# Kernel tuning notes

Hardware: AMD Instinct MI355X
Metric: run time of the kernel (lower is better)

Reference implementation:

```python
import jax, jax.numpy as jnp
import numpy as np

B, L, S, D_MODEL, H = 2, 2048, 2048, 1024, 16
D_HEAD = D_MODEL // H  # 64


def setup_inputs() -> dict:
    key = jax.random.key(0)
    ks = jax.random.split(key, 11)
    s = 0.02
    return {
        "queries": jax.random.normal(ks[0], (B, L, D_MODEL), jnp.float32),
        "keys": jax.random.normal(ks[1], (B, S, D_MODEL), jnp.float32),
        "values": jax.random.normal(ks[2], (B, S, D_MODEL), jnp.float32),
        # Linear weights stored as [in, out] (torch W.T), biases [out]
        "Wq": jax.random.normal(ks[3], (D_MODEL, H * D_HEAD), jnp.float32) * s,
        "bq": jnp.zeros((H * D_HEAD,), jnp.float32),
        "Wk": jax.random.normal(ks[4], (D_MODEL, H * D_HEAD), jnp.float32) * s,
        "bk": jnp.zeros((H * D_HEAD,), jnp.float32),
        "Wv": jax.random.normal(ks[5], (D_MODEL, H * D_HEAD), jnp.float32) * s,
        "bv": jnp.zeros((H * D_HEAD,), jnp.float32),
        "Wo": jax.random.normal(ks[6], (H * D_HEAD, D_MODEL), jnp.float32) * s,
        "bo": jnp.zeros((D_MODEL,), jnp.float32),
    }


def reference(queries, keys, values, Wq, bq, Wk, bk, Wv, bv, Wo, bo):
    b, l, _ = queries.shape
    _, s, _ = keys.shape
    # QKV projections -> [B, L/S, H, D_HEAD]
    q = (queries @ Wq + bq).reshape(b, l, H, D_HEAD)
    k = (keys @ Wk + bk).reshape(b, s, H, D_HEAD)
    v = (values @ Wv + bv).reshape(b, s, H, D_HEAD)
    scale = 1.0 / jnp.sqrt(jnp.asarray(D_HEAD, q.dtype))
    # Full score matrix [B, H, L, S] (mask_flag=False -> no causal mask)
    scores = jnp.einsum("blhe,bshe->bhls", q, k)
    A = jax.nn.softmax(scale * scores, axis=-1)  # dropout is identity at eval
    out = jnp.einsum("bhls,bshd->blhd", A, v).reshape(b, l, H * D_HEAD)
    out = out @ Wo + bo
    return out, A
```

## Files before the change

kernel.cpp:

```cpp
#include <hip/hip_runtime.h>


typedef __attribute__((ext_vector_type(8))) __bf16 bf16x8;
typedef __attribute__((ext_vector_type(4))) float f32x4;

__device__ __forceinline__ unsigned int f2bf_u(float f) {
  unsigned int u = __float_as_uint(f);
  return (u + 0x7FFFu + ((u >> 16) & 1u)) >> 16;
}
__device__ __forceinline__ float bf2f(unsigned int h) {
  return __uint_as_float(h << 16);
}
__device__ __forceinline__ unsigned int pack2(float lo, float hi) {
  return (f2bf_u(hi) << 16) | f2bf_u(lo);
}
__device__ __forceinline__ f32x4 mfma16(bf16x8 a, bf16x8 b, f32x4 c) {
  return __builtin_amdgcn_mfma_f32_16x16x32_bf16(a, b, c, 0, 0, 0);
}
__device__ __forceinline__ void gll16(const void* g, void* l) {
  __builtin_amdgcn_global_load_lds(
      (const __attribute__((address_space(1))) unsigned int*)g,
      (__attribute__((address_space(3))) unsigned int*)l, 16, 0, 0);
}

__global__ __launch_bounds__(256) void transpose_w(
    const float* __restrict__ W0, const float* __restrict__ W1,
    const float* __restrict__ W2, const float* __restrict__ W3,
    unsigned short* __restrict__ T0, unsigned short* __restrict__ T1,
    unsigned short* __restrict__ T2, unsigned short* __restrict__ T3) {
  const float* W; unsigned short* T;
  switch (blockIdx.z) {
    case 0: W = W0; T = T0; break;
    case 1: W = W1; T = T1; break;
    case 2: W = W2; T = T2; break;
    default: W = W3; T = T3; break;
  }
  __shared__ float tile[32][33];
  const int tx = threadIdx.x, ty = threadIdx.y;
  const int i0 = blockIdx.x * 32, o0 = blockIdx.y * 32;
  #pragma unroll
  for (int r = 0; r < 4; ++r)
    tile[ty + 8 * r][tx] = W[(size_t)(i0 + ty + 8 * r) * 1024 + o0 + tx];
  __syncthreads();
  #pragma unroll
  for (int r = 0; r < 4; ++r)
    T[(size_t)(o0 + ty + 8 * r) * 1024 + i0 + tx] =
        (unsigned short)f2bf_u(tile[tx][ty + 8 * r]);
}

struct GemmJob {
  const float* A;
  const unsigned short* BT;
  const float* bias;
  void* C;
  int omode;
};
struct GemmJobs { GemmJob j[3]; };

__global__ __launch_bounds__(256) void gemm_qkv(GemmJobs jobs, int M, int N, int K) {
  const GemmJob jb = jobs.j[blockIdx.z];
  __shared__ unsigned short As[128][40];
  __shared__ unsigned short Bs[128][32];
  const int tid = threadIdx.x;
  const int lane = tid & 63, wid = tid >> 6;
  const int l15 = lane & 15, l4 = lane >> 4;
  const int m0 = blockIdx.x * 128, n0 = blockIdx.y * 128;
  const int wr = wid >> 1, wc = wid & 1;

  f32x4 acc[4][4];
  #pragma unroll
  for (int i = 0; i < 4; ++i)
    #pragma unroll
    for (int j = 0; j < 4; ++j) acc[i][j] = (f32x4){0.f, 0.f, 0.f, 0.f};

  const int nk = K >> 5;
  for (int kt = 0; kt < nk; ++kt) {
    if (wid < 2) {
      #pragma unroll
      for (int c = 0; c < 8; ++c) {
        const int chunk = c * 128 + tid;
        const int row = chunk >> 3, col4 = chunk & 7;
        const float4 f = *(const float4*)(jb.A +
                                          (size_t)(m0 + row) * K + kt * 32 + col4 * 4);
        ushort4 o;
        o.x = (unsigned short)f2bf_u(f.x);
        o.y = (unsigned short)f2bf_u(f.y);
        o.z = (unsigned short)f2bf_u(f.z);
        o.w = (unsigned short)f2bf_u(f.w);
        *(ushort4*)&As[row][col4 * 4] = o;
      }
    } else {
      const int half = wid & 1;
      #pragma unroll
      for (int c = 0; c < 4; ++c) {
        const int off = half * 4096 + c * 1024;
        const int loff = off + lane * 16;
        const int row = loff >> 6, colb = loff & 63;
        gll16(jb.BT + (size_t)(n0 + row) * K + kt * 32 + colb / 2,
              (char*)&Bs[0][0] + off);
      }
    }
    __syncthreads();
    bf16x8 af[4], bfr[4];
    #pragma unroll
    for (int i = 0; i < 4; ++i)
      af[i] = *(const bf16x8*)&As[wr * 64 + i * 16 + l15][l4 * 8];
    #pragma unroll
    for (int j = 0; j < 4; ++j)
      bfr[j] = *(const bf16x8*)&Bs[wc * 64 + j * 16 + l15][l4 * 8];
    #pragma unroll
    for (int i = 0; i < 4; ++i)
      #pragma unroll
      for (int j = 0; j < 4; ++j)
        acc[i][j] = mfma16(af[i], bfr[j], acc[i][j]);
    __syncthreads();
  }

  #pragma unroll
  for (int j = 0; j < 4; ++j) {
    const int col = n0 + wc * 64 + j * 16 + l15;
    const float bv = jb.bias[col];
    #pragma unroll
    for (int i = 0; i < 4; ++i) {
      const int rowb = m0 + wr * 64 + i * 16 + l4 * 4;
      if (jb.omode == 2) {
        const int bq = rowb >> 11, sq = rowb & 2047;
        const int hq = col >> 6, dq = col & 63;
        ushort4 o;
        o.x = (unsigned short)f2bf_u(acc[i][j][0] + bv);
        o.y = (unsigned short)f2bf_u(acc[i][j][1] + bv);
        o.z = (unsigned short)f2bf_u(acc[i][j][2] + bv);
        o.w = (unsigned short)f2bf_u(acc[i][j][3] + bv);
        *(ushort4*)((unsigned short*)jb.C +
                    ((size_t)((bq * 16 + hq) * 64 + dq) << 11) + sq) = o;
      } else {
        #pragma unroll
        for (int q = 0; q < 4; ++q)
          ((unsigned short*)jb.C)[(size_t)(rowb + q) * N + col] =
              (unsigned short)f2bf_u(acc[i][j][q] + bv);
      }
    }
  }
}

__global__ __launch_bounds__(256) void gemm_out(
    const unsigned short* __restrict__ Ap, const unsigned short* __restrict__ BT,
    const float* __restrict__ bias, float* __restrict__ Cp,
    int M, int N, int K) {
  __shared__ unsigned short As[128][32];
  __shared__ unsigned short Bs[128][32];
  const int tid = threadIdx.x;
  const int lane = tid & 63, wid = tid >> 6;
  const int l15 = lane & 15, l4 = lane >> 4;
  const int m0 = blockIdx.x * 128, n0 = blockIdx.y * 128;
  const int wr = wid >> 1, wc = wid & 1;

  f32x4 acc[4][4];
  #pragma unroll
  for (int i = 0; i < 4; ++i)
    #pragma unroll
    for (int j = 0; j < 4; ++j) acc[i][j] = (f32x4){0.f, 0.f, 0.f, 0.f};

  const int nk = K >> 5;
  for (int kt = 0; kt < nk; ++kt) {
    const unsigned short* G = (wid < 2) ? (Ap + (size_t)m0 * K)
                                        : (BT + (size_t)n0 * K);
    char* L = (wid < 2) ? (char*)&As[0][0] : (char*)&Bs[0][0];
    const int half = wid & 1;
    #pragma unroll
    for (int c = 0; c < 4; ++c) {
      const int off = half * 4096 + c * 1024;
      const int loff = off + lane * 16;
      const int row = loff >> 6, colb = loff & 63;
      gll16(G + (size_t)row * K + kt * 32 + colb / 2, L + off);
    }
    __syncthreads();
    bf16x8 af[4], bfr[4];
    #pragma unroll
    for (int i = 0; i < 4; ++i)
      af[i] = *(const bf16x8*)&As[wr * 64 + i * 16 + l15][l4 * 8];
    #pragma unroll
    for (int j = 0; j < 4; ++j)
      bfr[j] = *(const bf16x8*)&Bs[wc * 64 + j * 16 + l15][l4 * 8];
    #pragma unroll
    for (int i = 0; i < 4; ++i)
      #pragma unroll
      for (int j = 0; j < 4; ++j)
        acc[i][j] = mfma16(af[i], bfr[j], acc[i][j]);
    __syncthreads();
  }

  #pragma unroll
  for (int j = 0; j < 4; ++j) {
    const int col = n0 + wc * 64 + j * 16 + l15;
    const float bv = bias[col];
    #pragma unroll
    for (int i = 0; i < 4; ++i) {
      const int rowb = m0 + wr * 64 + i * 16 + l4 * 4;
      #pragma unroll
      for (int q = 0; q < 4; ++q)
        Cp[(size_t)(rowb + q) * N + col] = acc[i][j][q] + bv;
    }
  }
}

__global__ __launch_bounds__(512) void attn_pv(
    const unsigned short* __restrict__ Q, const unsigned short* __restrict__ K,
    const unsigned short* __restrict__ VT, float2* __restrict__ Mst,
    unsigned short* __restrict__ OutPre) {
  __shared__ unsigned short Kt[128][64];
  __shared__ unsigned short Vt[64][128];

  const int tid = threadIdx.x;
  const int w = tid >> 6, lane = tid & 63;
  const int l15 = lane & 15, l4 = lane >> 4;
  const int wgid = blockIdx.x;
  const int xcd = wgid & 7, j = wgid >> 3;
  const int bh = xcd * 4 + (j >> 4);
  const int b = bh >> 4, h = bh & 15;
  const int m0 = (j & 15) * 128;

  const unsigned short* Qp =
      Q + ((size_t)(b * 2048 + m0 + w * 16 + l15) << 10) + h * 64 + l4 * 8;
  const bf16x8 qf0 = *(const bf16x8*)Qp;
  const bf16x8 qf1 = *(const bf16x8*)(Qp + 32);

  const unsigned short* Kb = K + ((size_t)b << 21) + h * 64;
  const unsigned short* Vbh = VT + ((size_t)bh << 17);

  const int krow = lane >> 3;
  const int kcolb = (lane & 7) ^ krow;
  const int vrow = lane >> 4;

  float m_run = -3.0e38f, l_run = 0.f;
  f32x4 pv[4];
  #pragma unroll
  for (int nt = 0; nt < 4; ++nt) pv[nt] = (f32x4){0.f, 0.f, 0.f, 0.f};

  for (int t = 0; t < 16; ++t) {
    #pragma unroll
    for (int c = 0; c < 2; ++c) {
      const int r = w * 16 + c * 8 + krow;
      gll16(Kb + ((size_t)(t * 128 + r) << 10) + kcolb * 8,
            &Kt[w * 16 + c * 8][0]);
    }
    #pragma unroll
    for (int c = 0; c < 2; ++c) {
      const int d = w * 8 + c * 4 + vrow;
      const int vc = (lane & 15) ^ (d & 7);
      gll16(Vbh + ((size_t)d << 11) + t * 128 + vc * 8,
            &Vt[w * 8 + c * 4][0]);
    }
    __syncthreads();

    unsigned int sc16[16];
    float tmax = -3.0e38f;
    #pragma unroll
    for (int sub = 0; sub < 8; ++sub) {
      const int row = sub * 16 + l15;
      const bf16x8 k0 = *(const bf16x8*)&Kt[row][(l4 ^ (l15 & 7)) * 8];
      const bf16x8 k1 = *(const bf16x8*)&Kt[row][((l4 + 4) ^ (l15 & 7)) * 8];
      f32x4 a = {0.f, 0.f, 0.f, 0.f};
      a = mfma16(k0, qf0, a);
      a = mfma16(k1, qf1, a);
      const unsigned int u0 = f2bf_u(a[0] * 0.125f);
      const unsigned int u1 = f2bf_u(a[1] * 0.125f);
      const unsigned int u2 = f2bf_u(a[2] * 0.125f);
      const unsigned int u3 = f2bf_u(a[3] * 0.125f);
      sc16[sub * 2 + 0] = (u1 << 16) | u0;
      sc16[sub * 2 + 1] = (u3 << 16) | u2;
      tmax = fmaxf(tmax, fmaxf(fmaxf(bf2f(u0), bf2f(u1)),
                               fmaxf(bf2f(u2), bf2f(u3))));
    }
    tmax = fmaxf(tmax, __shfl_xor(tmax, 16));
    tmax = fmaxf(tmax, __shfl_xor(tmax, 32));
    const float m_new = fmaxf(m_run, tmax);
    const float f = __expf(m_run - m_new);
    m_run = m_new;
    float fr[4];
    #pragma unroll
    for (int r = 0; r < 4; ++r) fr[r] = __shfl(f, l4 * 4 + r);
    #pragma unroll
    for (int nt = 0; nt < 4; ++nt) {
      pv[nt][0] *= fr[0]; pv[nt][1] *= fr[1];
      pv[nt][2] *= fr[2]; pv[nt][3] *= fr[3];
    }
    l_run *= f;

    union EF { unsigned int u4[4]; bf16x8 v; } ef[4];
    #pragma unroll
    for (int kc = 0; kc < 4; ++kc) {
      #pragma unroll
      for (int half = 0; half < 2; ++half) {
        const unsigned int p0 = sc16[(kc * 2 + half) * 2 + 0];
        const unsigned int p1 = sc16[(kc * 2 + half) * 2 + 1];
        const float e0 = __expf(bf2f(p0 & 0xffffu) - m_new);
        const float e1 = __expf(bf2f(p0 >> 16) - m_new);
        const float e2 = __expf(bf2f(p1 & 0xffffu) - m_new);
        const float e3 = __expf(bf2f(p1 >> 16) - m_new);
        l_run += e0 + e1 + e2 + e3;
        ef[kc].u4[half * 2 + 0] = pack2(e0, e1);
        ef[kc].u4[half * 2 + 1] = pack2(e2, e3);
      }
    }

    #pragma unroll
    for (int nt = 0; nt < 4; ++nt) {
      const int d = nt * 16 + l15;
      #pragma unroll
      for (int kc = 0; kc < 4; ++kc) {
        const int c16a = (kc * 4 + (l4 >> 1)) ^ (d & 7);
        const int c16b = (kc * 4 + 2 + (l4 >> 1)) ^ (d & 7);
        union { unsigned int u4[4]; bf16x8 v; } vf;
        const uint2 va = *(const uint2*)&Vt[d][c16a * 8 + (l4 & 1) * 4];
        const uint2 vb = *(const uint2*)&Vt[d][c16b * 8 + (l4 & 1) * 4];
        vf.u4[0] = va.x; vf.u4[1] = va.y; vf.u4[2] = vb.x; vf.u4[3] = vb.y;
        pv[nt] = mfma16(ef[kc].v, vf.v, pv[nt]);
      }
    }
    __syncthreads();
  }

  float lsum = l_run;
  lsum += __shfl_xor(lsum, 16);
  lsum += __shfl_xor(lsum, 32);
  const float linv = 1.0f / lsum;
  if (lane < 16)
    Mst[(size_t)bh * 2048 + m0 + w * 16 + lane] = make_float2(m_run, linv);
  #pragma unroll
  for (int r = 0; r < 4; ++r) {
    const float lq = __shfl(linv, l4 * 4 + r);
    const size_t rowoff =
        ((size_t)(b * 2048 + m0 + w * 16 + l4 * 4 + r) << 10) + h * 64;
    #pragma unroll
    for (int nt = 0; nt < 4; ++nt)
      OutPre[rowoff + nt * 16 + l15] =
          (unsigned short)f2bf_u(pv[nt][r] * lq);
  }
}

__global__ __launch_bounds__(512) void attn_awrite(
    const unsigned short* __restrict__ Q, const unsigned short* __restrict__ K,
    const float2* __restrict__ Mst, float* __restrict__ Aout) {
  __shared__ float atile[16][136];
  const int tid = threadIdx.x;
  const int w = tid >> 6, lane = tid & 63;
  const int l15 = lane & 15, l4 = lane >> 4;
  const int wgid = blockIdx.x;
  const int xcd = wgid & 7, j = wgid >> 3;
  const int bh = xcd * 4 + (j >> 7);
  const int b = bh >> 4, h = bh & 15;
  const int m0 = (j & 127) * 16;

  const unsigned short* Qp =
      Q + ((size_t)(b * 2048 + m0 + l15) << 10) + h * 64 + l4 * 8;
  const bf16x8 qf0 = *(const bf16x8*)Qp;
  const bf16x8 qf1 = *(const bf16x8*)(Qp + 32);
  const unsigned short* Kb = K + ((size_t)b << 21) + h * 64;

  const float2 ml = Mst[(size_t)bh * 2048 + m0 + l15];
  const float mreg = ml.x, lreg = ml.y;

  float* Awg = Aout + ((size_t)bh << 22) + ((size_t)m0 << 11);
  const int frow = tid >> 5;
  const int fcol = (tid & 31) * 4;

  const unsigned short* kp0 = Kb + ((size_t)(w * 16 + l15) << 10) + l4 * 8;
  bf16x8 ck0 = *(const bf16x8*)kp0;
  bf16x8 ck1 = *(const bf16x8*)(kp0 + 32);
  #pragma unroll
  for (int i = 0; i < 16; ++i) {
    bf16x8 nk0, nk1;
    if (i < 15) {
      const unsigned short* kp =
          Kb + ((size_t)((i + 1) * 128 + w * 16 + l15) << 10) + l4 * 8;
      nk0 = *(const bf16x8*)kp;
      nk1 = *(const bf16x8*)(kp + 32);
    }
    f32x4 a = {0.f, 0.f, 0.f, 0.f};
    a = mfma16(ck0, qf0, a);
    a = mfma16(ck1, qf1, a);
    ck0 = nk0;
    ck1 = nk1;
    f32x4 av;
    #pragma unroll
    for (int q = 0; q < 4; ++q) {
      const float sb = bf2f(f2bf_u(a[q] * 0.125f));
      av[q] = __expf(sb - mreg) * lreg;
    }
    *(f32x4*)&atile[l15][w * 16 + l4 * 4] = av;
    __syncthreads();
    const f32x4 v = *(const f32x4*)&atile[frow][fcol];
    __builtin_nontemporal_store(
        v, (f32x4*)(Awg + ((size_t)frow << 11) + i * 128 + fcol));
    __syncthreads();
  }
}

extern "C" void kernel_launch(void* const* d_in, const int* in_sizes, int n_in,
                              void* d_out, int out_size, void* d_ws,
                              size_t ws_size, hipStream_t stream) {
  (void)in_sizes; (void)n_in; (void)out_size; (void)ws_size;
  const float* queries = (const float*)d_in[0];
  const float* keys    = (const float*)d_in[1];
  const float* values  = (const float*)d_in[2];
  const float* Wq = (const float*)d_in[3];  const float* bq = (const float*)d_in[4];
  const float* Wk = (const float*)d_in[5];  const float* bk = (const float*)d_in[6];
  const float* Wv = (const float*)d_in[7];  const float* bv = (const float*)d_in[8];
  const float* Wo = (const float*)d_in[9];  const float* bo = (const float*)d_in[10];

  float* out  = (float*)d_out;
  float* Aout = out + (size_t)2 * 2048 * 1024;

  char* ws = (char*)d_ws;
  unsigned short* WqT = (unsigned short*)(ws + 0);
  unsigned short* WkT = (unsigned short*)(ws + 2097152);
  unsigned short* WvT = (unsigned short*)(ws + 4194304);
  unsigned short* WoT = (unsigned short*)(ws + 6291456);
  unsigned short* Qb  = (unsigned short*)(ws + 8388608);
  unsigned short* Kbf = (unsigned short*)(ws + 16777216);
  unsigned short* VTb = (unsigned short*)(ws + 25165824);
  unsigned short* Op  = (unsigned short*)(ws + 33554432);
  float2* Mst = (float2*)(ws + 41943040);

  transpose_w<<<dim3(32, 32, 4), dim3(32, 8), 0, stream>>>(
      Wq, Wk, Wv, Wo, WqT, WkT, WvT, WoT);

  GemmJobs qkv;
  qkv.j[0] = {queries, WqT, bq, Qb, 0};
  qkv.j[1] = {keys,    WkT, bk, Kbf, 0};
  qkv.j[2] = {values,  WvT, bv, VTb, 2};
  gemm_qkv<<<dim3(32, 8, 3), 256, 0, stream>>>(qkv, 4096, 1024, 1024);

  attn_pv<<<dim3(512), 512, 0, stream>>>(Qb, Kbf, VTb, Mst, Op);
  attn_awrite<<<dim3(4096), 512, 0, stream>>>(Qb, Kbf, Mst, Aout);

  gemm_out<<<dim3(32, 8), 256, 0, stream>>>(
      Op, WoT, bo, out, 4096, 1024, 1024);
}
```

Baseline: 300.6 us.

## Fuse output projection GEMM and attention-matrix write into one launch

Merges the output projection GEMM and the attention-probability write kernel into a single launch. The first 256 blocks run the GEMM and the rest write A, so the two independent tails can run at the same time and one launch gap goes away. The A-writer now uses 256 threads with 64-column tiles and 32 iterations instead of 512 threads with 128 columns, and shares LDS through a union. This doubles the number of barriers per row tile and mixes block types with different resource needs, which may affect occupancy.

```diff
diff --git a/kernel.cpp b/kernel.cpp
--- a/kernel.cpp
+++ b/kernel.cpp
@@ -143,67 +143,6 @@
   }
 }
 
-__global__ __launch_bounds__(256) void gemm_out(
-    const unsigned short* __restrict__ Ap, const unsigned short* __restrict__ BT,
-    const float* __restrict__ bias, float* __restrict__ Cp,
-    int M, int N, int K) {
-  __shared__ unsigned short As[128][32];
-  __shared__ unsigned short Bs[128][32];
-  const int tid = threadIdx.x;
-  const int lane = tid & 63, wid = tid >> 6;
-  const int l15 = lane & 15, l4 = lane >> 4;
-  const int m0 = blockIdx.x * 128, n0 = blockIdx.y * 128;
-  const int wr = wid >> 1, wc = wid & 1;
-
-  f32x4 acc[4][4];
-  #pragma unroll
-  for (int i = 0; i < 4; ++i)
-    #pragma unroll
-    for (int j = 0; j < 4; ++j) acc[i][j] = (f32x4){0.f, 0.f, 0.f, 0.f};
-
-  const int nk = K >> 5;
-  for (int kt = 0; kt < nk; ++kt) {
-    const unsigned short* G = (wid < 2) ? (Ap + (size_t)m0 * K)
-                                        : (BT + (size_t)n0 * K);
-    char* L = (wid < 2) ? (char*)&As[0][0] : (char*)&Bs[0][0];
-    const int half = wid & 1;
-    #pragma unroll
-    for (int c = 0; c < 4; ++c) {
-      const int off = half * 4096 + c * 1024;
-      const int loff = off + lane * 16;
-      const int row = loff >> 6, colb = loff & 63;
-      gll16(G + (size_t)row * K + kt * 32 + colb / 2, L + off);
-    }
-    __syncthreads();
-    bf16x8 af[4], bfr[4];
-    #pragma unroll
-    for (int i = 0; i < 4; ++i)
-      af[i] = *(const bf16x8*)&As[wr * 64 + i * 16 + l15][l4 * 8];
-    #pragma unroll
-    for (int j = 0; j < 4; ++j)
-      bfr[j] = *(const bf16x8*)&Bs[wc * 64 + j * 16 + l15][l4 * 8];
-    #pragma unroll
-    for (int i = 0; i < 4; ++i)
-      #pragma unroll
-      for (int j = 0; j < 4; ++j)
-        acc[i][j] = mfma16(af[i], bfr[j], acc[i][j]);
-    __syncthreads();
-  }
-
-  #pragma unroll
-  for (int j = 0; j < 4; ++j) {
-    const int col = n0 + wc * 64 + j * 16 + l15;
-    const float bv = bias[col];
-    #pragma unroll
-    for (int i = 0; i < 4; ++i) {
-      const int rowb = m0 + wr * 64 + i * 16 + l4 * 4;
-      #pragma unroll
-      for (int q = 0; q < 4; ++q)
-        Cp[(size_t)(rowb + q) * N + col] = acc[i][j][q] + bv;
-    }
-  }
-}
-
 __global__ __launch_bounds__(512) void attn_pv(
     const unsigned short* __restrict__ Q, const unsigned short* __restrict__ K,
     const unsigned short* __restrict__ VT, float2* __restrict__ Mst,
@@ -339,61 +278,123 @@
   }
 }
 
-__global__ __launch_bounds__(512) void attn_awrite(
+__global__ __launch_bounds__(256) void tail_fused(
+    const unsigned short* __restrict__ Op, const unsigned short* __restrict__ WoT,
+    const float* __restrict__ bo, float* __restrict__ Cout,
     const unsigned short* __restrict__ Q, const unsigned short* __restrict__ K,
     const float2* __restrict__ Mst, float* __restrict__ Aout) {
-  __shared__ float atile[16][136];
+  union SharedU {
+    struct { unsigned short As[128][32]; unsigned short Bs[128][32]; } g;
+    float atile[16][68];
+  };
+  __shared__ SharedU sh;
   const int tid = threadIdx.x;
-  const int w = tid >> 6, lane = tid & 63;
+  const int lane = tid & 63, wid = tid >> 6;
   const int l15 = lane & 15, l4 = lane >> 4;
-  const int wgid = blockIdx.x;
-  const int xcd = wgid & 7, j = wgid >> 3;
-  const int bh = xcd * 4 + (j >> 7);
-  const int b = bh >> 4, h = bh & 15;
-  const int m0 = (j & 127) * 16;
-
-  const unsigned short* Qp =
-      Q + ((size_t)(b * 2048 + m0 + l15) << 10) + h * 64 + l4 * 8;
-  const bf16x8 qf0 = *(const bf16x8*)Qp;
-  const bf16x8 qf1 = *(const bf16x8*)(Qp + 32);
-  const unsigned short* Kb = K + ((size_t)b << 21) + h * 64;
-
-  const float2 ml = Mst[(size_t)bh * 2048 + m0 + l15];
-  const float mreg = ml.x, lreg = ml.y;
-
-  float* Awg = Aout + ((size_t)bh << 22) + ((size_t)m0 << 11);
-  const int frow = tid >> 5;
-  const int fcol = (tid & 31) * 4;
-
-  const unsigned short* kp0 = Kb + ((size_t)(w * 16 + l15) << 10) + l4 * 8;
-  bf16x8 ck0 = *(const bf16x8*)kp0;
-  bf16x8 ck1 = *(const bf16x8*)(kp0 + 32);
-  #pragma unroll
-  for (int i = 0; i < 16; ++i) {
-    bf16x8 nk0, nk1;
-    if (i < 15) {
-      const unsigned short* kp =
-          Kb + ((size_t)((i + 1) * 128 + w * 16 + l15) << 10) + l4 * 8;
-      nk0 = *(const bf16x8*)kp;
-      nk1 = *(const bf16x8*)(kp + 32);
-    }
-    f32x4 a = {0.f, 0.f, 0.f, 0.f};
-    a = mfma16(ck0, qf0, a);
-    a = mfma16(ck1, qf1, a);
-    ck0 = nk0;
-    ck1 = nk1;
-    f32x4 av;
-    #pragma unroll
-    for (int q = 0; q < 4; ++q) {
-      const float sb = bf2f(f2bf_u(a[q] * 0.125f));
-      av[q] = __expf(sb - mreg) * lreg;
-    }
-    *(f32x4*)&atile[l15][w * 16 + l4 * 4] = av;
-    __syncthreads();
-    const f32x4 v = *(const f32x4*)&atile[frow][fcol];
-    __builtin_nontemporal_store(
-        v, (f32x4*)(Awg + ((size_t)frow << 11) + i * 128 + fcol));
-    __syncthreads();
+
+  if (blockIdx.x < 256) {
+    const int M = 4096, N = 1024, K_ = 1024;
+    const int m0 = (blockIdx.x >> 3) * 128, n0 = (blockIdx.x & 7) * 128;
+    const int wr = wid >> 1, wc = wid & 1;
+    (void)M;
+
+    f32x4 acc[4][4];
+    #pragma unroll
+    for (int i = 0; i < 4; ++i)
+      #pragma unroll
+      for (int j = 0; j < 4; ++j) acc[i][j] = (f32x4){0.f, 0.f, 0.f, 0.f};
+
+    for (int kt = 0; kt < (K_ >> 5); ++kt) {
+      const unsigned short* G = (wid < 2) ? (Op + (size_t)m0 * K_)
+                                          : (WoT + (size_t)n0 * K_);
+      char* L = (wid < 2) ? (char*)&sh.g.As[0][0] : (char*)&sh.g.Bs[0][0];
+      const int half = wid & 1;
+      #pragma unroll
+      for (int c = 0; c < 4; ++c) {
+        const int off = half * 4096 + c * 1024;
+        const int loff = off + lane * 16;
+        const int row = loff >> 6, colb = loff & 63;
+        gll16(G + (size_t)row * K_ + kt * 32 + colb / 2, L + off);
+      }
+      __syncthreads();
+      bf16x8 af[4], bfr[4];
+      #pragma unroll
+      for (int i = 0; i < 4; ++i)
+        af[i] = *(const bf16x8*)&sh.g.As[wr * 64 + i * 16 + l15][l4 * 8];
+      #pragma unroll
+      for (int j = 0; j < 4; ++j)
+        bfr[j] = *(const bf16x8*)&sh.g.Bs[wc * 64 + j * 16 + l15][l4 * 8];
+      #pragma unroll
+      for (int i = 0; i < 4; ++i)
+        #pragma unroll
+        for (int j = 0; j < 4; ++j)
+          acc[i][j] = mfma16(af[i], bfr[j], acc[i][j]);
+      __syncthreads();
+    }
+
+    #pragma unroll
+    for (int j = 0; j < 4; ++j) {
+      const int col = n0 + wc * 64 + j * 16 + l15;
+      const float bv = bo[col];
+      #pragma unroll
+      for (int i = 0; i < 4; ++i) {
+        const int rowb = m0 + wr * 64 + i * 16 + l4 * 4;
+        #pragma unroll
+        for (int q = 0; q < 4; ++q)
+          Cout[(size_t)(rowb + q) * N + col] = acc[i][j][q] + bv;
+      }
+    }
+  } else {
+    const int wgid = blockIdx.x - 256;
+    const int xcd = wgid & 7, j = wgid >> 3;
+    const int bh = xcd * 4 + (j >> 7);
+    const int b = bh >> 4, h = bh & 15;
+    const int m0 = (j & 127) * 16;
+    const int w = wid;
+
+    const unsigned short* Qp =
+        Q + ((size_t)(b * 2048 + m0 + l15) << 10) + h * 64 + l4 * 8;
+    const bf16x8 qf0 = *(const bf16x8*)Qp;
+    const bf16x8 qf1 = *(const bf16x8*)(Qp + 32);
+    const unsigned short* Kb = K + ((size_t)b << 21) + h * 64;
+
+    const float2 ml = Mst[(size_t)bh * 2048 + m0 + l15];
+    const float mreg = ml.x, lreg = ml.y;
+
+    float* Awg = Aout + ((size_t)bh << 22) + ((size_t)m0 << 11);
+    const int frow = tid >> 4;
+    const int fcol = (tid & 15) * 4;
+
+    const unsigned short* kp0 = Kb + ((size_t)(w * 16 + l15) << 10) + l4 * 8;
+    bf16x8 ck0 = *(const bf16x8*)kp0;
+    bf16x8 ck1 = *(const bf16x8*)(kp0 + 32);
+    #pragma unroll 8
+    for (int i = 0; i < 32; ++i) {
+      bf16x8 nk0, nk1;
+      if (i < 31) {
+        const unsigned short* kp =
+            Kb + ((size_t)((i + 1) * 64 + w * 16 + l15) << 10) + l4 * 8;
+        nk0 = *(const bf16x8*)kp;
+        nk1 = *(const bf16x8*)(kp + 32);
+      }
+      f32x4 a = {0.f, 0.f, 0.f, 0.f};
+      a = mfma16(ck0, qf0, a);
+      a = mfma16(ck1, qf1, a);
+      ck0 = nk0;
+      ck1 = nk1;
+      f32x4 av;
+      #pragma unroll
+      for (int q = 0; q < 4; ++q) {
+        const float sb = bf2f(f2bf_u(a[q] * 0.125f));
+        av[q] = __expf(sb - mreg) * lreg;
+      }
+      *(f32x4*)&sh.atile[l15][w * 16 + l4 * 4] = av;
+      __syncthreads();
+      const f32x4 v = *(const f32x4*)&sh.atile[frow][fcol];
+      __builtin_nontemporal_store(
+          v, (f32x4*)(Awg + ((size_t)frow << 11) + i * 64 + fcol));
+      __syncthreads();
+    }
   }
 }
 
@@ -433,8 +434,7 @@
   gemm_qkv<<<dim3(32, 8, 3), 256, 0, stream>>>(qkv, 4096, 1024, 1024);
 
   attn_pv<<<dim3(512), 512, 0, stream>>>(Qb, Kbf, VTb, Mst, Op);
-  attn_awrite<<<dim3(4096), 512, 0, stream>>>(Qb, Kbf, Mst, Aout);
-
-  gemm_out<<<dim3(32, 8), 256, 0, stream>>>(
-      Op, WoT, bo, out, 4096, 1024, 1024);
-}
+
+  tail_fused<<<dim3(4352), 256, 0, stream>>>(
+      Op, WoT, bo, out, Qb, Kbf, Mst, Aout);
+}
```

After: 322.6 us. 7.3% more time.
